# Kernel optimization log

Hardware: AMD Instinct MI355X
Metric: run time of the kernel (lower is better)

The kernel has to match this reference:

```python
import jax, jax.numpy as jnp
import numpy as np

N, E, H, L, OUT, PDIM, NREL = 50000, 400000, 512, 4, 250, 2, 3
SLOPE = 0.2  # LeakyReLU negative slope


def leaky(x):
    return jnp.where(x > 0, x, SLOPE * x)


def seg_mean(msg, idx, n):
    # scatter-mean of per-edge messages onto destination nodes
    s = jax.ops.segment_sum(msg, idx, num_segments=n)
    c = jax.ops.segment_sum(jnp.ones((idx.shape[0], 1), msg.dtype), idx, num_segments=n)
    return s / jnp.maximum(c, 1.0)


def setup_inputs() -> dict:
    key = jax.random.key(0)
    ks = jax.random.split(key, 18)
    w = lambda k, shape: jax.random.normal(k, shape, dtype=jnp.float32) * 0.05
    return {
        "x_window": jax.random.normal(ks[0], (N, H), dtype=jnp.float32),
        "x_pos": jax.random.normal(ks[1], (N, PDIM), dtype=jnp.float32),
        "edge_near": jax.random.randint(ks[2], (2, E), 0, N),
        "edge_close": jax.random.randint(ks[3], (2, E), 0, N),
        "edge_sim": jax.random.randint(ks[4], (2, E), 0, N),
        "W_pre": w(ks[5], (H, H)),            # pretransform_win (no bias)
        "W_post": w(ks[6], (H, H)),           # post_plot_transform linear (no bias)
        "Wl": w(ks[7], (L, NREL, H, H)),      # SAGE neighbor transform per layer/relation
        "Wr": w(ks[8], (L, NREL, H, H)),      # SAGE self transform per layer/relation
        "Wpos": w(ks[9], (L, NREL, PDIM, H)), # edge_embed: relative-position embedding
        "Wg": w(ks[10], (L, H, H)),           # global vector injection per layer
        "seed": w(ks[11], (L, H)),            # GMPool_I seed query per layer
        "Wk": w(ks[12], (L, H, H)),
        "Wv": w(ks[13], (L, H, H)),
        "W_out": w(ks[14], (H, OUT)),
        "b_out": jnp.zeros((OUT,), jnp.float32),
    }


def reference(x_window, x_pos, edge_near, edge_close, edge_sim,
              W_pre, W_post, Wl, Wr, Wpos, Wg, seed, Wk, Wv, W_out, b_out):
    edges = (edge_near, edge_close, edge_sim)
    # pretransform + post_plot_transform: LeakyReLU -> Linear -> LeakyReLU
    x = leaky(leaky(x_window @ W_pre) @ W_post)
    inv_sqrt = np.float32(1.0 / np.sqrt(H))
    for l in range(L):
        # GMPool_I attention pooling over all nodes -> one global vector [H]
        attn = jax.nn.softmax(((x @ Wk[l]) @ seed[l]) * inv_sqrt)  # [N]
        g = attn @ (x @ Wv[l])                                      # [H]
        gterm = g @ Wg[l]                                           # [H]
        acc = jnp.zeros_like(x)
        for r in range(NREL):
            src, dst = edges[r][0], edges[r][1]
            # message = neighbor feature + relative-position edge embedding
            msg = x[src] + (x_pos[src] - x_pos[dst]) @ Wpos[l, r]   # [E,H]
            agg = seg_mean(msg, dst, N)                             # [N,H]
            acc = acc + agg @ Wl[l, r] + x @ Wr[l, r] + gterm
        x = leaky(acc / np.float32(NREL))  # HeteroConv aggr='mean' + LeakyReLU
    return x @ W_out + b_out
```

## Files before the change

### kernel.cpp

```cpp
#include <hip/hip_runtime.h>

#define NN 50000
#define EE 400000
#define HH 512
#define LL 4
#define OUTC 250
#define MP 50048
#define HH2 (HH*HH)
#define NPW 512
#define NBLK 49
#define INV_SQRT_H 0.044194173824159216f

typedef unsigned short u16;
typedef __attribute__((ext_vector_type(8))) unsigned short u16x8;
typedef __attribute__((ext_vector_type(8))) short s16x8;
typedef __attribute__((ext_vector_type(4))) float f32x4;

__device__ __forceinline__ float b2f(u16 v) {
  union { unsigned u; float f; } c; c.u = ((unsigned)v) << 16; return c.f;
}
__device__ __forceinline__ u16 f2b(float f) {
  union { float f; unsigned u; } c; c.f = f;
  unsigned r = c.u + 0x7fffu + ((c.u >> 16) & 1u);
  return (u16)(r >> 16);
}
__device__ __forceinline__ float leakyf(float v) { return v > 0.f ? v : 0.2f * v; }

__device__ __forceinline__ void async16(const void* g, void* l) {
  __builtin_amdgcn_global_load_lds((const __attribute__((address_space(1))) void*)g,
                                   (__attribute__((address_space(3))) void*)l,
                                   16, 0, 0);
}

__global__ void k_hist(const int* __restrict__ e0, const int* __restrict__ e1,
                       const int* __restrict__ e2, int* __restrict__ cnt) {
  int r = blockIdx.y;
  const int* dst = (r == 0 ? e0 : r == 1 ? e1 : e2) + EE;
  int i = blockIdx.x * 256 + threadIdx.x;
  if (i < EE) atomicAdd(&cnt[r * NN + dst[i]], 1);
}

__global__ void k_scan1(const int* __restrict__ cnt, int* __restrict__ offs,
                        float* __restrict__ invc, int* __restrict__ bsum) {
  int r = blockIdx.y, b = blockIdx.x, t = threadIdx.x;
  int i = b * 1024 + t;
  int v = (i < NN) ? cnt[r * NN + i] : 0;
  __shared__ int sm[1024];
  sm[t] = v;
  __syncthreads();
#pragma unroll
  for (int d = 1; d < 1024; d <<= 1) {
    int u = (t >= d) ? sm[t - d] : 0;
    __syncthreads();
    sm[t] += u;
    __syncthreads();
  }
  if (i < NN) {
    offs[r * (NN + 1) + i] = sm[t] - v;
    invc[r * NN + i] = 1.f / (float)(v > 1 ? v : 1);
  }
  if (t == 1023) bsum[r * NBLK + b] = sm[t];
}

__global__ void k_scan2(int* __restrict__ bsum) {
  int t = threadIdx.x;
  int r = t >> 6, lane = t & 63;
  if (r >= 3) return;
  int orig = (lane < NBLK) ? bsum[r * NBLK + lane] : 0;
  int v = orig;
#pragma unroll
  for (int d = 1; d < 64; d <<= 1) {
    int u = __shfl_up(v, d);
    if (lane >= d) v += u;
  }
  if (lane < NBLK) bsum[r * NBLK + lane] = v - orig;
}

__global__ void k_scan3(const int* __restrict__ bsum, int* __restrict__ offs,
                        int* __restrict__ cursor) {
  int r = blockIdx.y, b = blockIdx.x, t = threadIdx.x;
  int i = b * 1024 + t;
  if (i < NN) {
    int v = offs[r * (NN + 1) + i] + bsum[r * NBLK + b];
    offs[r * (NN + 1) + i] = v;
    cursor[r * NN + i] = v;
  }
  if (b == 0 && t == 0) offs[r * (NN + 1) + NN] = EE;
}

__global__ void k_fill(const int* __restrict__ e0, const int* __restrict__ e1,
                       const int* __restrict__ e2,
                       int* __restrict__ cursor, int* __restrict__ csr) {
  int r = blockIdx.y;
  const int* ep = (r == 0 ? e0 : r == 1 ? e1 : e2);
  int i = blockIdx.x * 256 + threadIdx.x;
  if (i >= EE) return;
  int s = ep[i], d = ep[EE + i];
  int slot = atomicAdd(&cursor[r * NN + d], 1);
  csr[r * EE + slot] = s;
}

__global__ void k_pvec(const int* __restrict__ offs, const int* __restrict__ csr,
                       const float2* __restrict__ pos, float* __restrict__ P) {
  int r = blockIdx.y;
  int i = blockIdx.x * 256 + threadIdx.x;
  if (i >= NN) return;
  const int* o = offs + r * (NN + 1);
  const int* cs = csr + (size_t)r * EE;
  int b = o[i], e = o[i + 1];
  float sx = 0.f, sy = 0.f;
  for (int k = b; k < e; ++k) {
    float2 p = pos[cs[k]];
    sx += p.x; sy += p.y;
  }
  float2 pd = pos[i];
  float c = (float)(e - b);
  P[(size_t)r * NN * 2 + 2 * i]     = sx - c * pd.x;
  P[(size_t)r * NN * 2 + 2 * i + 1] = sy - c * pd.y;
}

__global__ void k_transT14(const float* __restrict__ Wl, const float* __restrict__ W_pre,
                           const float* __restrict__ W_post,
                           u16* __restrict__ wlT, u16* __restrict__ wpreT,
                           u16* __restrict__ wpostT) {
  __shared__ float sm[32][33];
  int z = blockIdx.z;
  const float* Wm; u16* WTm;
  if (z < 12)      { Wm = Wl + (size_t)z * HH2;  WTm = wlT + (size_t)z * HH2; }
  else if (z == 12){ Wm = W_pre;                  WTm = wpreT; }
  else             { Wm = W_post;                 WTm = wpostT; }
  int r0 = blockIdx.y * 32, c0 = blockIdx.x * 32;
  int tx = threadIdx.x, ty = threadIdx.y;
#pragma unroll
  for (int i = 0; i < 4; ++i)
    sm[ty + i * 8][tx] = Wm[(size_t)(r0 + ty + i * 8) * HH + c0 + tx];
  __syncthreads();
#pragma unroll
  for (int i = 0; i < 4; ++i)
    WTm[(size_t)(c0 + ty + i * 8) * HH + r0 + tx] = f2b(sm[tx][ty + i * 8]);
}

__global__ void k_sum3T(const float* __restrict__ Wr, u16* __restrict__ WT) {
  __shared__ float sm[32][33];
  int l = blockIdx.z;
  const float* W3 = Wr + (size_t)l * 3 * HH2;
  u16* WTm = WT + (size_t)l * HH2;
  int r0 = blockIdx.y * 32, c0 = blockIdx.x * 32;
  int tx = threadIdx.x, ty = threadIdx.y;
#pragma unroll
  for (int i = 0; i < 4; ++i) {
    size_t idx = (size_t)(r0 + ty + i * 8) * HH + c0 + tx;
    sm[ty + i * 8][tx] = W3[idx] + W3[HH2 + idx] + W3[2 * (size_t)HH2 + idx];
  }
  __syncthreads();
#pragma unroll
  for (int i = 0; i < 4; ++i)
    WTm[(size_t)(c0 + ty + i * 8) * HH + r0 + tx] = f2b(sm[tx][ty + i * 8]);
}

__global__ void k_transpose_pad(const float* __restrict__ W, u16* __restrict__ WT,
                                int rows, int cols, int tcols) {
  int idx = blockIdx.x * 256 + threadIdx.x;
  if (idx >= rows * tcols) return;
  int r = idx % rows, c = idx / rows;
  float v = (c < cols) ? W[(size_t)r * cols + c] : 0.f;
  WT[(size_t)c * rows + r] = f2b(v);
}

#define CVT_BLK ((NN * HH / 8 + 255) / 256)
__global__ void k_cvt_zero(const float* __restrict__ in, u16* __restrict__ out,
                           u16* a, u16* b, u16* c, u16* d, u16* e) {
  int blk = blockIdx.x;
  if (blk < CVT_BLK) {
    int i = blk * 256 + threadIdx.x;
    if (i >= NN * HH / 8) return;
    const float4 x = *(const float4*)(in + (size_t)i * 8);
    const float4 y = *(const float4*)(in + (size_t)i * 8 + 4);
    u16x8 o;
    o[0] = f2b(x.x); o[1] = f2b(x.y); o[2] = f2b(x.z); o[3] = f2b(x.w);
    o[4] = f2b(y.x); o[5] = f2b(y.y); o[6] = f2b(y.z); o[7] = f2b(y.w);
    *(u16x8*)(out + (size_t)i * 8) = o;
  } else {
    int i = (blk - CVT_BLK) * 256 + threadIdx.x;
    const int per = (MP - NN) * HH;
    if (i >= per * 5) return;
    int sel = i / per, rem = i - sel * per;
    u16* p = sel == 0 ? a : sel == 1 ? b : sel == 2 ? c : sel == 3 ? d : e;
    p[(size_t)NN * HH + rem] = 0;
  }
}

__global__ void k_kvec(const float* __restrict__ Wk, const float* __restrict__ seed,
                       float* __restrict__ kvec) {
  int l = blockIdx.x;
  const float* Wkl = Wk + (size_t)l * HH2;
  const float* sdl = seed + (size_t)l * HH;
  float* kv = kvec + (size_t)l * HH;
  int w = threadIdx.x >> 6, lane = threadIdx.x & 63;
  float sv[8];
#pragma unroll
  for (int i = 0; i < 8; ++i) sv[i] = sdl[lane * 8 + i];
  for (int row = w; row < HH; row += 8) {
    const float* p = Wkl + (size_t)row * HH + lane * 8;
    float d = 0.f;
#pragma unroll
    for (int i = 0; i < 8; ++i) d += p[i] * sv[i];
#pragma unroll
    for (int o = 32; o > 0; o >>= 1) d += __shfl_xor(d, o);
    if (lane == 0) kv[row] = d;
  }
}

__global__ void k_pool2g(const float* __restrict__ part, const float* __restrict__ Wv,
                         const float* __restrict__ Wg, float* __restrict__ gterm) {
  __shared__ float red[512];
  __shared__ float gv[HH];
  __shared__ float g[HH];
  int t = threadIdx.x;
  red[t] = part[(size_t)t * 514];
  __syncthreads();
  for (int s = 256; s > 0; s >>= 1) {
    if (t < s) red[t] = fmaxf(red[t], red[t + s]);
    __syncthreads();
  }
  float M = red[0];
  float s = 0.f, z = 0.f;
  for (int w = 0; w < NPW; ++w) {
    const float* p = part + (size_t)w * 514;
    float e = __expf(p[0] - M);
    z += e * p[1];
    s += e * p[2 + t];
  }
  gv[t] = s / z;
  __syncthreads();
  float a = 0.f;
  for (int i = 0; i < HH; ++i) a += gv[i] * Wv[(size_t)i * HH + t];
  g[t] = a;
  __syncthreads();
  float b = 0.f;
  for (int i = 0; i < HH; ++i) b += g[i] * Wg[(size_t)i * HH + t];
  gterm[t] = b;
}

__global__ void k_spmm_pool(const int* __restrict__ offs, const int* __restrict__ csr,
                            const float* __restrict__ invc, const float* __restrict__ P,
                            const float* __restrict__ wposL, const u16* __restrict__ x,
                            u16* __restrict__ agg, const float* __restrict__ kvec,
                            float* __restrict__ part) {
  int r = blockIdx.y;
  int lane = threadIdx.x & 63;
  if (r == 3) {
    if (blockIdx.x >= NPW / 4) return;
    int gw = (blockIdx.x * 256 + threadIdx.x) >> 6;
    float kl[8];
#pragma unroll
    for (int i = 0; i < 8; ++i) kl[i] = kvec[lane * 8 + i];
    float m = -1e30f, Z = 0.f;
    float acc[8] = {0, 0, 0, 0, 0, 0, 0, 0};
    for (int n = gw; n < NN; n += NPW) {
      u16x8 v = *(const u16x8*)(x + (size_t)n * HH + lane * 8);
      float xl[8], d = 0.f;
#pragma unroll
      for (int i = 0; i < 8; ++i) { xl[i] = b2f(v[i]); d += xl[i] * kl[i]; }
#pragma unroll
      for (int o = 32; o > 0; o >>= 1) d += __shfl_xor(d, o);
      d *= INV_SQRT_H;
      float mn = fmaxf(m, d);
      float c = __expf(m - mn), w = __expf(d - mn);
      Z = Z * c + w;
#pragma unroll
      for (int i = 0; i < 8; ++i) acc[i] = acc[i] * c + w * xl[i];
      m = mn;
    }
    float* p = part + (size_t)gw * 514;
#pragma unroll
    for (int i = 0; i < 8; ++i) p[2 + lane * 8 + i] = acc[i];
    if (lane == 0) { p[0] = m; p[1] = Z; }
    return;
  }
  int wv = (blockIdx.x * 256 + threadIdx.x) >> 6;
  if (wv >= NN) return;
  const int* o = offs + r * (NN + 1);
  const int* cs = csr + (size_t)r * EE;
  const float* wpos = wposL + (size_t)r * 2 * HH;
  int beg = o[wv], end = o[wv + 1];
  float acc[8] = {0, 0, 0, 0, 0, 0, 0, 0};
  int k = beg;
  for (; k + 3 < end; k += 4) {
    int s0 = cs[k], s1 = cs[k + 1], s2 = cs[k + 2], s3 = cs[k + 3];
    u16x8 v0 = *(const u16x8*)(x + (size_t)s0 * HH + lane * 8);
    u16x8 v1 = *(const u16x8*)(x + (size_t)s1 * HH + lane * 8);
    u16x8 v2 = *(const u16x8*)(x + (size_t)s2 * HH + lane * 8);
    u16x8 v3 = *(const u16x8*)(x + (size_t)s3 * HH + lane * 8);
#pragma unroll
    for (int i = 0; i < 8; ++i)
      acc[i] += (b2f(v0[i]) + b2f(v1[i])) + (b2f(v2[i]) + b2f(v3[i]));
  }
  for (; k < end; ++k) {
    int s0 = cs[k];
    u16x8 v0 = *(const u16x8*)(x + (size_t)s0 * HH + lane * 8);
#pragma unroll
    for (int i = 0; i < 8; ++i) acc[i] += b2f(v0[i]);
  }
  float px = P[(size_t)r * NN * 2 + 2 * wv], py = P[(size_t)r * NN * 2 + 2 * wv + 1];
  float ic = invc[(size_t)r * NN + wv];
  u16x8 out;
#pragma unroll
  for (int i = 0; i < 8; ++i) {
    float w0 = wpos[lane * 8 + i];
    float w1 = wpos[HH + lane * 8 + i];
    float v = (acc[i] + px * w0 + py * w1) * ic;
    out[i] = f2b(v);
  }
  __builtin_nontemporal_store(out, (u16x8*)(agg + ((size_t)r * MP + wv) * HH + lane * 8));
}

__global__ __launch_bounds__(256) void k_gemm(
    const u16* __restrict__ A0, const u16* __restrict__ A1,
    const u16* __restrict__ A2, const u16* __restrict__ A3,
    const u16* __restrict__ B0, const u16* __restrict__ B1,
    const u16* __restrict__ B2, const u16* __restrict__ B3,
    int nkt, int mode, float alpha, const float* __restrict__ gvec,
    u16* __restrict__ outB, float* __restrict__ outF,
    const float* __restrict__ bias, int M, int Nout, int G, int gx)
{
  __shared__ u16 lsA[128 * 64];
  __shared__ u16 lsB[128 * 64];
  const int tid = threadIdx.x;
  const int wave = tid >> 6, lane = tid & 63;
  const int wm = (wave >> 1) * 64, wn = (wave & 1) * 64;

  const int gid = blockIdx.x;
  const int q = G >> 3, rr = G & 7;
  const int xk = gid & 7, idx = gid >> 3;
  const int tl = xk * q + (xk < rr ? xk : rr) + idx;
  const int rowM0 = (tl / gx) * 128, colN0 = (tl % gx) * 128;

  f32x4 acc[4][4];
#pragma unroll
  for (int i = 0; i < 4; ++i)
#pragma unroll
    for (int j = 0; j < 4; ++j) acc[i][j] = (f32x4){0.f, 0.f, 0.f, 0.f};

  const int rowT = wave * 8 + (lane >> 3);
  const int c8 = lane & 7;
  int aoff[2][4], boff[2][4];
#pragma unroll
  for (int K0 = 0; K0 < 2; ++K0)
#pragma unroll
    for (int f = 0; f < 4; ++f) {
      const int cb = K0 * 4 + (lane >> 4);
      const int mm = wm + f * 16 + (lane & 15);
      const int nn = wn + f * 16 + (lane & 15);
      aoff[K0][f] = mm * 64 + ((cb ^ (mm & 7)) << 3);
      boff[K0][f] = nn * 64 + ((cb ^ (nn & 7)) << 3);
    }

  const int nkb = nkt >> 3;
  for (int kb = 0; kb < nkb; ++kb) {
    const u16* As = kb == 0 ? A0 : (kb == 1 ? A1 : (kb == 2 ? A2 : A3));
    const u16* Bs = kb == 0 ? B0 : (kb == 1 ? B1 : (kb == 2 ? B2 : B3));
    for (int k8 = 0; k8 < 8; ++k8) {
      const int koff = k8 * 64;
#pragma unroll
      for (int i = 0; i < 4; ++i) {
        const int r = i * 32 + rowT;
        const int scol = (c8 ^ (r & 7)) * 8;
        async16(As + (size_t)(rowM0 + r) * HH + koff + scol, &lsA[i * 2048 + wave * 512]);
        async16(Bs + (size_t)(colN0 + r) * HH + koff + scol, &lsB[i * 2048 + wave * 512]);
      }
      __syncthreads();
#pragma unroll
      for (int K0 = 0; K0 < 2; ++K0) {
        s16x8 af[4], bfr[4];
#pragma unroll
        for (int f = 0; f < 4; ++f) {
          af[f] = *(const s16x8*)&lsA[aoff[K0][f]];
          bfr[f] = *(const s16x8*)&lsB[boff[K0][f]];
        }
#pragma unroll
        for (int fm = 0; fm < 4; ++fm)
#pragma unroll
          for (int fn = 0; fn < 4; ++fn)
            acc[fm][fn] = __builtin_amdgcn_mfma_f32_16x16x32_bf16(af[fm], bfr[fn], acc[fm][fn], 0, 0, 0);
      }
      __syncthreads();
    }
  }

#pragma unroll
  for (int fm = 0; fm < 4; ++fm) {
#pragma unroll
    for (int fn = 0; fn < 4; ++fn) {
#pragma unroll
      for (int r = 0; r < 4; ++r) {
        const int row = rowM0 + wm + fm * 16 + ((lane >> 4) << 2) + r;
        const int col = colN0 + wn + fn * 16 + (lane & 15);
        float v = acc[fm][fn][r];
        if (mode == 0) {
          v = v * alpha + (gvec ? gvec[col] : 0.f);
          __builtin_nontemporal_store(f2b(leakyf(v)), &outB[(size_t)row * HH + col]);
        } else {
          if (row < M && col < Nout)
            __builtin_nontemporal_store(v + (bias ? bias[col] : 0.f), &outF[(size_t)row * Nout + col]);
        }
      }
    }
  }
}

extern "C" void kernel_launch(void* const* d_in, const int* in_sizes, int n_in,
                              void* d_out, int out_size, void* d_ws, size_t ws_size,
                              hipStream_t stream) {
  (void)in_sizes; (void)n_in; (void)out_size;
  const float* x_window = (const float*)d_in[0];
  const float* x_pos    = (const float*)d_in[1];
  const int*   e0 = (const int*)d_in[2];
  const int*   e1 = (const int*)d_in[3];
  const int*   e2 = (const int*)d_in[4];
  const float* W_pre  = (const float*)d_in[5];
  const float* W_post = (const float*)d_in[6];
  const float* Wl   = (const float*)d_in[7];
  const float* Wr   = (const float*)d_in[8];
  const float* Wpos = (const float*)d_in[9];
  const float* Wg   = (const float*)d_in[10];
  const float* seed = (const float*)d_in[11];
  const float* Wk   = (const float*)d_in[12];
  const float* Wv   = (const float*)d_in[13];
  const float* W_out= (const float*)d_in[14];
  const float* b_out= (const float*)d_in[15];
  float* out = (float*)d_out;

  char* base = (char*)d_ws;
  size_t off = 0;
  auto alloc = [&](size_t bytes) -> char* {
    char* p = base + off;
    off += (bytes + 255) & ~(size_t)255;
    return p;
  };
  u16* x_a   = (u16*)alloc((size_t)MP * HH * 2);
  u16* x_b   = (u16*)alloc((size_t)MP * HH * 2);
  u16* agg0  = (u16*)alloc((size_t)MP * HH * 2);
  u16* agg1  = (u16*)alloc((size_t)MP * HH * 2);
  u16* agg2  = (u16*)alloc((size_t)MP * HH * 2);
  u16* wlT   = (u16*)alloc((size_t)12 * HH2 * 2);
  u16* wrsT  = (u16*)alloc((size_t)4 * HH2 * 2);
  u16* wpreT = (u16*)alloc((size_t)HH2 * 2);
  u16* wpostT= (u16*)alloc((size_t)HH2 * 2);
  u16* woutT = (u16*)alloc((size_t)256 * HH * 2);
  int* offs  = (int*)alloc((size_t)3 * (NN + 1) * 4);
  int* curs  = (int*)alloc((size_t)3 * NN * 4);
  int* cnt   = (int*)alloc((size_t)3 * NN * 4);
  int* csr   = (int*)alloc((size_t)3 * EE * 4);
  float* invc = (float*)alloc((size_t)3 * NN * 4);
  float* P    = (float*)alloc((size_t)3 * NN * 2 * 4);
  float* kvec  = (float*)alloc((size_t)LL * HH * 4);
  float* gterm = (float*)alloc(HH * 4);
  int* bsum  = (int*)alloc((size_t)3 * NBLK * 4);
  float* part  = (float*)curs;
  if (off > ws_size) return;

  hipMemsetAsync(cnt, 0, (size_t)3 * NN * 4, stream);

  k_hist<<<dim3((EE + 255) / 256, 3), 256, 0, stream>>>(e0, e1, e2, cnt);
  k_scan1<<<dim3(NBLK, 3), 1024, 0, stream>>>(cnt, offs, invc, bsum);
  k_scan2<<<1, 256, 0, stream>>>(bsum);
  k_scan3<<<dim3(NBLK, 3), 1024, 0, stream>>>(bsum, offs, curs);
  k_fill<<<dim3((EE + 255) / 256, 3), 256, 0, stream>>>(e0, e1, e2, curs, csr);
  k_pvec<<<dim3((NN + 255) / 256, 3), 256, 0, stream>>>(offs, csr, (const float2*)x_pos, P);

  k_transT14<<<dim3(16, 16, 14), dim3(32, 8), 0, stream>>>(Wl, W_pre, W_post,
                                                           wlT, wpreT, wpostT);
  k_sum3T<<<dim3(16, 16, 4), dim3(32, 8), 0, stream>>>(Wr, wrsT);
  k_transpose_pad<<<(HH * 256) / 256, 256, 0, stream>>>(W_out, woutT, HH, OUTC, 256);
  k_kvec<<<LL, 512, 0, stream>>>(Wk, seed, kvec);

  const int padBlk = ((MP - NN) * HH * 5 + 255) / 256;
  k_cvt_zero<<<CVT_BLK + padBlk, 256, 0, stream>>>(x_window, x_b, x_a, x_b, agg0, agg1, agg2);

  const u16* nul = nullptr;
  const int G4 = 4 * (MP / 128), G2 = 2 * (MP / 128);
  k_gemm<<<G4, 256, 0, stream>>>(x_b, nul, nul, nul, wpreT, nul, nul, nul,
                                 8, 0, 1.f, nullptr, agg0, nullptr, nullptr, NN, HH, G4, 4);
  k_gemm<<<G4, 256, 0, stream>>>(agg0, nul, nul, nul, wpostT, nul, nul, nul,
                                 8, 0, 1.f, nullptr, x_a, nullptr, nullptr, NN, HH, G4, 4);

  u16* cur = x_a; u16* nxt = x_b;
  for (int l = 0; l < LL; ++l) {
    k_spmm_pool<<<dim3(NN / 4, 4), 256, 0, stream>>>(offs, csr, invc, P,
                                                     Wpos + (size_t)l * 3 * 2 * HH, cur, agg0,
                                                     kvec + (size_t)l * HH, part);
    k_pool2g<<<1, 512, 0, stream>>>(part, Wv + (size_t)l * HH2, Wg + (size_t)l * HH2, gterm);
    k_gemm<<<G4, 256, 0, stream>>>(
        agg0, agg1, agg2, cur,
        wlT + (size_t)(l * 3 + 0) * HH2, wlT + (size_t)(l * 3 + 1) * HH2,
        wlT + (size_t)(l * 3 + 2) * HH2, wrsT + (size_t)l * HH2,
        32, 0, (1.f / 3.f), gterm, nxt, nullptr, nullptr, NN, HH, G4, 4);
    u16* t = cur; cur = nxt; nxt = t;
  }
  k_gemm<<<G2, 256, 0, stream>>>(cur, nul, nul, nul, woutT, nul, nul, nul,
                                 8, 1, 1.f, nullptr, nullptr, out, b_out, NN, OUTC, G2, 2);
}
```

Measured before the change: 2.339 ms.

## Gather neighbor features from an FP8 copy of x in SpMM

The GEMM epilogue now also writes an FP8 (e4m3) copy of each layer's node features. The SpMM aggregation gathers neighbor rows from that copy, which halves the gather bytes, and its inner loop is unrolled to 8 edges. The aim is to cut the memory traffic of the random neighbor gathers, which dominate the aggregation kernel. In exchange, messages lose precision to FP8, which may hurt accuracy, and the GEMM epilogue gains extra single-byte stores.

```diff
diff --git a/kernel.cpp b/kernel.cpp
--- a/kernel.cpp
+++ b/kernel.cpp
@@ -12,9 +12,11 @@
 #define INV_SQRT_H 0.044194173824159216f
 
 typedef unsigned short u16;
+typedef unsigned char u8;
 typedef __attribute__((ext_vector_type(8))) unsigned short u16x8;
 typedef __attribute__((ext_vector_type(8))) short s16x8;
 typedef __attribute__((ext_vector_type(4))) float f32x4;
+typedef __attribute__((ext_vector_type(2))) float f32x2;
 
 __device__ __forceinline__ float b2f(u16 v) {
   union { unsigned u; float f; } c; c.u = ((unsigned)v) << 16; return c.f;
@@ -242,9 +244,19 @@
   gterm[t] = b;
 }
 
+__device__ __forceinline__ void acc_fp8x8(float* acc, uint2 v) {
+  f32x2 a0 = __builtin_amdgcn_cvt_pk_f32_fp8(v.x, false);
+  f32x2 a1 = __builtin_amdgcn_cvt_pk_f32_fp8(v.x, true);
+  f32x2 a2 = __builtin_amdgcn_cvt_pk_f32_fp8(v.y, false);
+  f32x2 a3 = __builtin_amdgcn_cvt_pk_f32_fp8(v.y, true);
+  acc[0] += a0[0]; acc[1] += a0[1]; acc[2] += a1[0]; acc[3] += a1[1];
+  acc[4] += a2[0]; acc[5] += a2[1]; acc[6] += a3[0]; acc[7] += a3[1];
+}
+
 __global__ void k_spmm_pool(const int* __restrict__ offs, const int* __restrict__ csr,
                             const float* __restrict__ invc, const float* __restrict__ P,
                             const float* __restrict__ wposL, const u16* __restrict__ x,
+                            const u8* __restrict__ x8,
                             u16* __restrict__ agg, const float* __restrict__ kvec,
                             float* __restrict__ part) {
   int r = blockIdx.y;
@@ -278,7 +290,7 @@
     if (lane == 0) { p[0] = m; p[1] = Z; }
     return;
   }
-  int wv = (blockIdx.x * 256 + threadIdx.x) >> 6;
+  int wv = __builtin_amdgcn_readfirstlane((int)(blockIdx.x * 256 + threadIdx.x) >> 6);
   if (wv >= NN) return;
   const int* o = offs + r * (NN + 1);
   const int* cs = csr + (size_t)r * EE;
@@ -286,21 +298,29 @@
   int beg = o[wv], end = o[wv + 1];
   float acc[8] = {0, 0, 0, 0, 0, 0, 0, 0};
   int k = beg;
+  for (; k + 7 < end; k += 8) {
+    int s[8];
+#pragma unroll
+    for (int j = 0; j < 8; ++j) s[j] = cs[k + j];
+    uint2 v[8];
+#pragma unroll
+    for (int j = 0; j < 8; ++j) v[j] = *(const uint2*)(x8 + (size_t)s[j] * HH + lane * 8);
+#pragma unroll
+    for (int j = 0; j < 8; ++j) acc_fp8x8(acc, v[j]);
+  }
   for (; k + 3 < end; k += 4) {
-    int s0 = cs[k], s1 = cs[k + 1], s2 = cs[k + 2], s3 = cs[k + 3];
-    u16x8 v0 = *(const u16x8*)(x + (size_t)s0 * HH + lane * 8);
-    u16x8 v1 = *(const u16x8*)(x + (size_t)s1 * HH + lane * 8);
-    u16x8 v2 = *(const u16x8*)(x + (size_t)s2 * HH + lane * 8);
-    u16x8 v3 = *(const u16x8*)(x + (size_t)s3 * HH + lane * 8);
-#pragma unroll
-    for (int i = 0; i < 8; ++i)
-      acc[i] += (b2f(v0[i]) + b2f(v1[i])) + (b2f(v2[i]) + b2f(v3[i]));
+    int s[4];
+#pragma unroll
+    for (int j = 0; j < 4; ++j) s[j] = cs[k + j];
+    uint2 v[4];
+#pragma unroll
+    for (int j = 0; j < 4; ++j) v[j] = *(const uint2*)(x8 + (size_t)s[j] * HH + lane * 8);
+#pragma unroll
+    for (int j = 0; j < 4; ++j) acc_fp8x8(acc, v[j]);
   }
   for (; k < end; ++k) {
-    int s0 = cs[k];
-    u16x8 v0 = *(const u16x8*)(x + (size_t)s0 * HH + lane * 8);
-#pragma unroll
-    for (int i = 0; i < 8; ++i) acc[i] += b2f(v0[i]);
+    uint2 v0 = *(const uint2*)(x8 + (size_t)cs[k] * HH + lane * 8);
+    acc_fp8x8(acc, v0);
   }
   float px = P[(size_t)r * NN * 2 + 2 * wv], py = P[(size_t)r * NN * 2 + 2 * wv + 1];
   float ic = invc[(size_t)r * NN + wv];
@@ -321,7 +341,7 @@
     const u16* __restrict__ B0, const u16* __restrict__ B1,
     const u16* __restrict__ B2, const u16* __restrict__ B3,
     int nkt, int mode, float alpha, const float* __restrict__ gvec,
-    u16* __restrict__ outB, float* __restrict__ outF,
+    u16* __restrict__ outB, u8* __restrict__ out8, float* __restrict__ outF,
     const float* __restrict__ bias, int M, int Nout, int G, int gx)
 {
   __shared__ u16 lsA[128 * 64];
@@ -398,8 +418,12 @@
         const int col = colN0 + wn + fn * 16 + (lane & 15);
         float v = acc[fm][fn][r];
         if (mode == 0) {
-          v = v * alpha + (gvec ? gvec[col] : 0.f);
-          __builtin_nontemporal_store(f2b(leakyf(v)), &outB[(size_t)row * HH + col]);
+          v = leakyf(v * alpha + (gvec ? gvec[col] : 0.f));
+          __builtin_nontemporal_store(f2b(v), &outB[(size_t)row * HH + col]);
+          if (out8) {
+            int pk = __builtin_amdgcn_cvt_pk_fp8_f32(v, v, 0, false);
+            __builtin_nontemporal_store((u8)pk, &out8[(size_t)row * HH + col]);
+          }
         } else {
           if (row < M && col < Nout)
             __builtin_nontemporal_store(v + (bias ? bias[col] : 0.f), &outF[(size_t)row * Nout + col]);
@@ -443,6 +467,7 @@
   u16* agg0  = (u16*)alloc((size_t)MP * HH * 2);
   u16* agg1  = (u16*)alloc((size_t)MP * HH * 2);
   u16* agg2  = (u16*)alloc((size_t)MP * HH * 2);
+  u8*  x8    = (u8*)alloc((size_t)MP * HH);
   u16* wlT   = (u16*)alloc((size_t)12 * HH2 * 2);
   u16* wrsT  = (u16*)alloc((size_t)4 * HH2 * 2);
   u16* wpreT = (u16*)alloc((size_t)HH2 * 2);
@@ -481,23 +506,23 @@
   const u16* nul = nullptr;
   const int G4 = 4 * (MP / 128), G2 = 2 * (MP / 128);
   k_gemm<<<G4, 256, 0, stream>>>(x_b, nul, nul, nul, wpreT, nul, nul, nul,
-                                 8, 0, 1.f, nullptr, agg0, nullptr, nullptr, NN, HH, G4, 4);
+                                 8, 0, 1.f, nullptr, agg0, nullptr, nullptr, nullptr, NN, HH, G4, 4);
   k_gemm<<<G4, 256, 0, stream>>>(agg0, nul, nul, nul, wpostT, nul, nul, nul,
-                                 8, 0, 1.f, nullptr, x_a, nullptr, nullptr, NN, HH, G4, 4);
+                                 8, 0, 1.f, nullptr, x_a, x8, nullptr, nullptr, NN, HH, G4, 4);
 
   u16* cur = x_a; u16* nxt = x_b;
   for (int l = 0; l < LL; ++l) {
     k_spmm_pool<<<dim3(NN / 4, 4), 256, 0, stream>>>(offs, csr, invc, P,
-                                                     Wpos + (size_t)l * 3 * 2 * HH, cur, agg0,
+                                                     Wpos + (size_t)l * 3 * 2 * HH, cur, x8, agg0,
                                                      kvec + (size_t)l * HH, part);
     k_pool2g<<<1, 512, 0, stream>>>(part, Wv + (size_t)l * HH2, Wg + (size_t)l * HH2, gterm);
     k_gemm<<<G4, 256, 0, stream>>>(
         agg0, agg1, agg2, cur,
         wlT + (size_t)(l * 3 + 0) * HH2, wlT + (size_t)(l * 3 + 1) * HH2,
         wlT + (size_t)(l * 3 + 2) * HH2, wrsT + (size_t)l * HH2,
-        32, 0, (1.f / 3.f), gterm, nxt, nullptr, nullptr, NN, HH, G4, 4);
+        32, 0, (1.f / 3.f), gterm, nxt, (l < LL - 1) ? x8 : nullptr, nullptr, nullptr, NN, HH, G4, 4);
     u16* t = cur; cur = nxt; nxt = t;
   }
   k_gemm<<<G2, 256, 0, stream>>>(cur, nul, nul, nul, woutT, nul, nul, nul,
-                                 8, 1, 1.f, nullptr, nullptr, out, b_out, NN, OUTC, G2, 2);
-}
+                                 8, 1, 1.f, nullptr, nullptr, nullptr, out, b_out, NN, OUTC, G2, 2);
+}
```

New measurement: 2.317 ms. About the same (-0.9%).
